# Kernel optimization log

Hardware: AMD Instinct MI355X
Metric: run time of the kernel (lower is better)

## Reference

```python
import jax, jax.numpy as jnp
import numpy as np

MODEL_DIM = 1024
NUM_HEADS = 16
D_K = MODEL_DIM // NUM_HEADS  # 64
MAX_SEQ_LEN = 3200
B, T = 2, 2048
THETA_BASE = 10000.0


def setup_inputs() -> dict:
    key = jax.random.key(0)
    ks = jax.random.split(key, 5)
    scale = 1.0 / np.sqrt(MODEL_DIM)
    x = jax.random.normal(ks[0], (B, T, MODEL_DIM), dtype=jnp.float32)
    wq = jax.random.normal(ks[1], (MODEL_DIM, MODEL_DIM), dtype=jnp.float32) * scale
    wk = jax.random.normal(ks[2], (MODEL_DIM, MODEL_DIM), dtype=jnp.float32) * scale
    wv = jax.random.normal(ks[3], (MODEL_DIM, MODEL_DIM), dtype=jnp.float32) * scale
    wo = jax.random.normal(ks[4], (MODEL_DIM, MODEL_DIM), dtype=jnp.float32) * scale
    bq = jnp.zeros((MODEL_DIM,), jnp.float32)
    bk = jnp.zeros((MODEL_DIM,), jnp.float32)
    bv = jnp.zeros((MODEL_DIM,), jnp.float32)
    bo = jnp.zeros((MODEL_DIM,), jnp.float32)
    # RoPE tables, exactly as precompute_rotation_matrix: theta duplicated
    # adjacently ([t0,t0,t1,t1,...]).
    theta = THETA_BASE ** (jnp.arange(D_K // 2, dtype=jnp.float32) * (-2.0 / D_K))
    ang = jnp.outer(jnp.arange(MAX_SEQ_LEN, dtype=jnp.float32), theta)  # [L, d/2]
    ang = jnp.repeat(ang, 2, axis=-1)  # [L, d]
    return {
        "x": x, "wq": wq, "bq": bq, "wk": wk, "bk": bk,
        "wv": wv, "bv": bv, "wo": wo, "bo": bo,
        "cos": jnp.cos(ang), "sin": jnp.sin(ang),
    }


def reference(x, wq, bq, wk, bk, wv, bv, wo, bo, cos, sin):
    b, t, dm = x.shape
    h, d = NUM_HEADS, dm // NUM_HEADS

    # NOTE: original uses .view(b, h, t, d) directly on [b, t, h*d] (no
    # transpose) — a nonstandard head split we replicate faithfully.
    xq = (x @ wq.T + bq).reshape(b, h, t, d)
    xk = (x @ wk.T + bk).reshape(b, h, t, d)
    xv = (x @ wv.T + bv).reshape(b, h, t, d)

    def rot_half(q):
        # pairs are adjacent (2i, 2i+1): out[2i] = -q[2i+1], out[2i+1] = q[2i]
        q2 = q.reshape(b, h, t, d // 2, 2)
        return jnp.stack([-q2[..., 1], q2[..., 0]], axis=-1).reshape(b, h, t, d)

    # NOTE: original indexes cos/sin at the single position `seq_len`
    # (rotation_matrix_cos[:, :, xq.shape[2], :]), broadcasting one row over
    # all positions — replicated faithfully.
    c = cos[t]  # [d]
    s = sin[t]  # [d]
    xq = xq * c + rot_half(xq) * s
    xk = xk * c + rot_half(xk) * s

    scores = jnp.einsum("bhqd,bhkd->bhqk", xq, xk) / np.sqrt(d)
    p = jax.nn.softmax(scores, axis=-1)  # mask='none', dropout=0.0
    o = jnp.einsum("bhqk,bhkd->bhqd", p, xv)
    o = o.transpose(0, 2, 1, 3).reshape(b, t, dm)  # 'b h t d -> b t (h d)'
    return o @ wo.T + bo
```

## Files before the change

### kernel.cpp

```cpp
#include <hip/hip_runtime.h>

typedef _Float16 half8 __attribute__((ext_vector_type(8)));
typedef __fp16 pkh2 __attribute__((ext_vector_type(2)));
typedef float floatx4 __attribute__((ext_vector_type(4)));

#define AS1 __attribute__((address_space(1)))
#define AS3 __attribute__((address_space(3)))


__global__ __launch_bounds__(256) void convert_kernel(
    const float* __restrict__ x, const float* __restrict__ wq,
    const float* __restrict__ wk, const float* __restrict__ wv,
    const float* __restrict__ wo,
    _Float16* __restrict__ xb, _Float16* __restrict__ wqkv,
    _Float16* __restrict__ wob)
{
    int i = (blockIdx.x * 256 + threadIdx.x) * 4;
    const float* src; _Float16* dst; int off;
    if (i < 4194304)      { src = x;  dst = xb;            off = i; }
    else if (i < 5242880) { src = wq; dst = wqkv;          off = i - 4194304; }
    else if (i < 6291456) { src = wk; dst = wqkv + 1048576; off = i - 5242880; }
    else if (i < 7340032) { src = wv; dst = wqkv + 2097152; off = i - 6291456; }
    else                  { src = wo; dst = wob;           off = i - 7340032; }
    float4 v = *(const float4*)(src + off);
    union { uint2 u; pkh2 h[2]; } o;
    o.h[0] = __builtin_amdgcn_cvt_pkrtz(v.x, v.y);
    o.h[1] = __builtin_amdgcn_cvt_pkrtz(v.z, v.w);
    *(uint2*)(dst + off) = o.u;
}

template<bool QKV, int BM>
__global__ __launch_bounds__(256) void gemm_kernel(
    const _Float16* __restrict__ A, const _Float16* __restrict__ W,
    const float* __restrict__ b0, const float* __restrict__ b1,
    const float* __restrict__ b2,
    const float* __restrict__ cosr, const float* __restrict__ sinr,
    _Float16* __restrict__ O0, _Float16* __restrict__ O1,
    _Float16* __restrict__ O2, float* __restrict__ Of)
{
    constexpr int MT = BM / 32;
    __shared__ __align__(16) _Float16 As[BM * 64];
    __shared__ __align__(16) _Float16 Bs[128 * 64];
    const int tid  = threadIdx.x;
    const int lane = tid & 63, w = tid >> 6;
    const int lrow = lane & 15, quad = lane >> 4;
    const int wr = (w & 1) * (BM / 2), wc = (w >> 1) * 64;
    const int arow0 = blockIdx.x * BM;
    const int brow0 = blockIdx.y * 128;

    const int r8 = lane >> 3;
    const int gcol = ((lane & 7) ^ r8) * 8;

    floatx4 acc[MT][4] = {};

    for (int kk = 0; kk < 1024; kk += 64) {
        __syncthreads();
        for (int u = 0; u < MT; u++) {
            const int row = w * (8 * MT) + u * 8;
            __builtin_amdgcn_global_load_lds(
                (const AS1 unsigned*)(const void*)(A + (size_t)(arow0 + row + r8) * 1024 + kk + gcol),
                (AS3 unsigned*)(void*)(As + row * 64), 16, 0, 0);
        }
        for (int u = 0; u < 4; u++) {
            const int row = w * 32 + u * 8;
            __builtin_amdgcn_global_load_lds(
                (const AS1 unsigned*)(const void*)(W + (size_t)(brow0 + row + r8) * 1024 + kk + gcol),
                (AS3 unsigned*)(void*)(Bs + row * 64), 16, 0, 0);
        }
        __syncthreads();
        for (int ks = 0; ks < 2; ks++) {
            const int swz = ((ks * 4 + quad) ^ (lrow & 7)) * 8;
            half8 af[MT], bf[4];
            for (int mt = 0; mt < MT; mt++)
                af[mt] = *(const half8*)&As[(wr + mt * 16 + lrow) * 64 + swz];
            for (int nt = 0; nt < 4; nt++)
                bf[nt] = *(const half8*)&Bs[(wc + nt * 16 + lrow) * 64 + swz];
            for (int mt = 0; mt < MT; mt++)
                for (int nt = 0; nt < 4; nt++)
                    acc[mt][nt] = __builtin_amdgcn_mfma_f32_16x16x32_f16(
                        af[mt], bf[nt], acc[mt][nt], 0, 0, 0);
        }
    }

    if (QKV) {
        const int seg = blockIdx.y >> 3;
        const float* bias = seg == 0 ? b0 : (seg == 1 ? b1 : b2);
        _Float16* out = seg == 0 ? O0 : (seg == 1 ? O1 : O2);
        const int nbase = (blockIdx.y & 7) * 128 + wc;
        for (int nt = 0; nt < 4; nt++) {
            const int n = nbase + nt * 16 + lrow;
            const float bv = bias[n];
            const int dj = n & 63;
            const float cv = cosr[dj], sv = sinr[dj];
            const bool odd = (n & 1) != 0;
            const int ns = (seg == 1)
                ? ((n & ~56) | ((((n >> 3) ^ (n >> 6)) & 7) << 3))
                : n;
            for (int mt = 0; mt < MT; mt++)
                for (int r = 0; r < 4; r++) {
                    float v = acc[mt][nt][r] + bv;
                    if (seg < 2) {
                        float p = __shfl_xor(v, 1, 64);
                        v = odd ? (v * cv + p * sv) : (v * cv - p * sv);
                    }
                    if (seg == 0) v *= 0.125f;
                    int row = arow0 + wr + mt * 16 + quad * 4 + r;
                    out[row * 1024 + ns] = (_Float16)v;
                }
        }
    } else {
        const int nbase = blockIdx.y * 128 + wc;
        for (int nt = 0; nt < 4; nt++) {
            const int n = nbase + nt * 16 + lrow;
            const float bv = b0[n];
            for (int mt = 0; mt < MT; mt++)
                for (int r = 0; r < 4; r++) {
                    int row = arow0 + wr + mt * 16 + quad * 4 + r;
                    Of[row * 1024 + n] = acc[mt][nt][r] + bv;
                }
        }
    }
}

__global__ __launch_bounds__(256) void vtrans_kernel(
    const _Float16* __restrict__ V, _Float16* __restrict__ VT)
{
    __shared__ __align__(16) _Float16 T[64][72];
    const int tid = threadIdx.x;
    const int kt = blockIdx.x;
    const int bh = blockIdx.y;
    const int bi = bh >> 4, hi = bh & 15;
    const _Float16* Vh = V + (size_t)(bi * 2048 + hi * 128) * 1024 + kt * 4096;
    const int srow = tid >> 3, sblk = tid & 7;
    union { uint4 u; _Float16 h[8]; } a, b;
    a.u = *(const uint4*)(Vh + (2 * srow) * 64 + sblk * 8);
    b.u = *(const uint4*)(Vh + (2 * srow + 1) * 64 + sblk * 8);
    for (int j = 0; j < 8; j++) {
        union { unsigned u; _Float16 h[2]; } pk;
        pk.h[0] = a.h[j]; pk.h[1] = b.h[j];
        *(unsigned*)&T[sblk * 8 + j][2 * srow] = pk.u;
    }
    __syncthreads();
    const int d = tid >> 2, c = tid & 3;
    const int xr = d & 7;
    _Float16* outrow = VT + ((size_t)bh * 64 + d) * 2048 + kt * 64;
    *(uint4*)(outrow + ((2 * c)     ^ xr) * 8) = *(const uint4*)&T[d][c * 16];
    *(uint4*)(outrow + ((2 * c + 1) ^ xr) * 8) = *(const uint4*)&T[d][c * 16 + 8];
}

static __device__ __forceinline__ half8 assemble_p(uint2 a, uint2 b) {
    auto s32x = __builtin_amdgcn_permlane32_swap(a.x, b.x, false, false);
    auto s32y = __builtin_amdgcn_permlane32_swap(a.y, b.y, false, false);
    auto s16x = __builtin_amdgcn_permlane16_swap(s32x[0], s32x[1], false, false);
    auto s16y = __builtin_amdgcn_permlane16_swap(s32y[0], s32y[1], false, false);
    union { uint4 u; half8 h; } r;
    r.u.x = s16x[0];
    r.u.y = s16y[0];
    r.u.z = s16x[1];
    r.u.w = s16y[1];
    return r.h;
}

__global__ __launch_bounds__(512, 4) void attn_kernel(
    const _Float16* __restrict__ Q, const _Float16* __restrict__ K,
    const _Float16* __restrict__ VT, _Float16* __restrict__ O)
{
    __shared__ __align__(16) _Float16 smem[26624];

    const int tid  = threadIdx.x;
    const int g    = tid >> 8;
    const int t8   = tid & 255;
    const int wg   = tid >> 6;
    const int w    = wg & 3;
    const int lane = tid & 63;
    const int lrow = lane & 15, quad = lane >> 4;

    const int bid = blockIdx.x;
    const int bh  = (bid & 7) * 4 + (bid >> 7);
    const int qt  = (bid >> 3) & 15;
    const int bi = bh >> 4, hi = bh & 15;
    const size_t base = (size_t)(bi * 2048 + hi * 128) * 1024;
    const _Float16* Qh  = Q + base;
    const _Float16* Kh  = K + base + (size_t)g * 65536;
    const _Float16* VTh = VT + (size_t)bh * 131072 + g * 1024;

    _Float16* Ksg  = smem + g * 4096;
    _Float16* Vtsg = smem + 8192 + g * 4096;

    half8 qf[2][2];
    for (int nt = 0; nt < 2; nt++)
        for (int ks = 0; ks < 2; ks++)
            qf[nt][ks] = *(const half8*)(Qh + (qt * 128 + w * 32 + nt * 16 + lrow) * 64
                                          + ks * 32 + quad * 8);

    floatx4 oacc[4][2] = {};
    float lsum0 = 0.0f, lsum1 = 0.0f;

    const int srow = t8 >> 3, sblk = t8 & 7;
    const int vd = t8 >> 2;
    const int vq0 = (2 * (t8 & 3)) ^ (vd & 7);
    const int vq1 = vq0 ^ 1;
    const _Float16* vrow = VTh + (size_t)vd * 2048;

    uint4 k0 = *(const uint4*)(Kh + srow * 64 + sblk * 8);
    uint4 k1 = *(const uint4*)(Kh + (srow + 32) * 64 + sblk * 8);
    uint4 v0 = *(const uint4*)(vrow + vq0 * 8);
    uint4 v1 = *(const uint4*)(vrow + vq1 * 8);

    const float LOG2E = 1.44269504f;
    const float OFF   = -8.65617025f;

    for (int ktl = 0; ktl < 16; ktl++) {
        __syncthreads();
        *(uint4*)&Ksg[srow * 64 + sblk * 8]        = k0;
        *(uint4*)&Ksg[(srow + 32) * 64 + sblk * 8] = k1;
        *(uint4*)&Vtsg[vd * 64 + vq0 * 8] = v0;
        *(uint4*)&Vtsg[vd * 64 + vq1 * 8] = v1;
        if (ktl < 15) {
            const _Float16* Kt = Kh + (ktl + 1) * 4096;
            k0 = *(const uint4*)(Kt + srow * 64 + sblk * 8);
            k1 = *(const uint4*)(Kt + (srow + 32) * 64 + sblk * 8);
            const _Float16* Vt = vrow + (ktl + 1) * 64;
            v0 = *(const uint4*)(Vt + vq0 * 8);
            v1 = *(const uint4*)(Vt + vq1 * 8);
        }
        __syncthreads();
        for (int h = 0; h < 2; h++) {
            union { uint2 u; pkh2 h2[2]; } pA[2], pB[2];
            for (int k2 = 0; k2 < 2; k2++) {
                const int kt4 = h * 2 + k2;
                floatx4 s0 = {}, s1 = {};
                for (int ks = 0; ks < 2; ks++) {
                    half8 af = *(const half8*)&Ksg[(kt4 * 16 + lrow) * 64
                                 + (((ks * 4 + quad) ^ (lrow & 7)) * 8)];
                    s0 = __builtin_amdgcn_mfma_f32_16x16x32_f16(af, qf[0][ks], s0, 0, 0, 0);
                    s1 = __builtin_amdgcn_mfma_f32_16x16x32_f16(af, qf[1][ks], s1, 0, 0, 0);
                }
                float p00 = __builtin_amdgcn_exp2f(fmaf(s0[0], LOG2E, OFF));
                float p01 = __builtin_amdgcn_exp2f(fmaf(s0[1], LOG2E, OFF));
                float p02 = __builtin_amdgcn_exp2f(fmaf(s0[2], LOG2E, OFF));
                float p03 = __builtin_amdgcn_exp2f(fmaf(s0[3], LOG2E, OFF));
                float p10 = __builtin_amdgcn_exp2f(fmaf(s1[0], LOG2E, OFF));
                float p11 = __builtin_amdgcn_exp2f(fmaf(s1[1], LOG2E, OFF));
                float p12 = __builtin_amdgcn_exp2f(fmaf(s1[2], LOG2E, OFF));
                float p13 = __builtin_amdgcn_exp2f(fmaf(s1[3], LOG2E, OFF));
                lsum0 += (p00 + p01) + (p02 + p03);
                lsum1 += (p10 + p11) + (p12 + p13);
                pA[k2].h2[0] = __builtin_amdgcn_cvt_pkrtz(p00, p01);
                pA[k2].h2[1] = __builtin_amdgcn_cvt_pkrtz(p02, p03);
                pB[k2].h2[0] = __builtin_amdgcn_cvt_pkrtz(p10, p11);
                pB[k2].h2[1] = __builtin_amdgcn_cvt_pkrtz(p12, p13);
            }
            half8 bf0 = assemble_p(pA[0].u, pA[1].u);
            half8 bf1 = assemble_p(pB[0].u, pB[1].u);
            for (int dt = 0; dt < 4; dt++) {
                half8 av = *(const half8*)&Vtsg[(dt * 16 + lrow) * 64
                              + (((h * 4 + quad) ^ (lrow & 7)) * 8)];
                oacc[dt][0] = __builtin_amdgcn_mfma_f32_16x16x32_f16(av, bf0, oacc[dt][0], 0, 0, 0);
                oacc[dt][1] = __builtin_amdgcn_mfma_f32_16x16x32_f16(av, bf1, oacc[dt][1], 0, 0, 0);
            }
        }
    }
    __syncthreads();

    float* X = (float*)smem;
    float* L = (float*)(smem + 16384);
    if (g == 1) {
        for (int dt = 0; dt < 4; dt++)
            for (int nt = 0; nt < 2; nt++)
                *(floatx4*)&X[((dt * 2 + nt) * 256 + w * 64 + lane) * 4] = oacc[dt][nt];
        L[(w * 64 + lane) * 2]     = lsum0;
        L[(w * 64 + lane) * 2 + 1] = lsum1;
    }
    __syncthreads();
    if (g == 0) {
        for (int dt = 0; dt < 4; dt++)
            for (int nt = 0; nt < 2; nt++)
                oacc[dt][nt] += *(const floatx4*)&X[((dt * 2 + nt) * 256 + w * 64 + lane) * 4];
        lsum0 += L[(w * 64 + lane) * 2];
        lsum1 += L[(w * 64 + lane) * 2 + 1];
        lsum0 += __shfl_xor(lsum0, 16, 64); lsum0 += __shfl_xor(lsum0, 32, 64);
        lsum1 += __shfl_xor(lsum1, 16, 64); lsum1 += __shfl_xor(lsum1, 32, 64);
        const float inv0 = 1.0f / lsum0, inv1 = 1.0f / lsum1;
        _Float16* Es = smem + 17408 + w * 2304;
        for (int dt = 0; dt < 4; dt++) {
            union { uint2 u; pkh2 h2[2]; } a0, a1;
            a0.h2[0] = __builtin_amdgcn_cvt_pkrtz(oacc[dt][0][0] * inv0, oacc[dt][0][1] * inv0);
            a0.h2[1] = __builtin_amdgcn_cvt_pkrtz(oacc[dt][0][2] * inv0, oacc[dt][0][3] * inv0);
            a1.h2[0] = __builtin_amdgcn_cvt_pkrtz(oacc[dt][1][0] * inv1, oacc[dt][1][1] * inv1);
            a1.h2[1] = __builtin_amdgcn_cvt_pkrtz(oacc[dt][1][2] * inv1, oacc[dt][1][3] * inv1);
            *(uint2*)&Es[lrow * 72 + dt * 16 + quad * 4]        = a0.u;
            *(uint2*)&Es[(16 + lrow) * 72 + dt * 16 + quad * 4] = a1.u;
        }
        const int rw = lane >> 1, hf = lane & 1;
        const size_t orow = (size_t)(bi * 2048 + qt * 128 + w * 32 + rw) * 1024
                            + hi * 64 + hf * 32;
        for (int i = 0; i < 4; i++)
            *(uint4*)(O + orow + i * 8) = *(const uint4*)&Es[rw * 72 + hf * 32 + i * 8];
    }
}

extern "C" void kernel_launch(void* const* d_in, const int* in_sizes, int n_in,
                              void* d_out, int out_size, void* d_ws, size_t ws_size,
                              hipStream_t stream) {
    const float* x    = (const float*)d_in[0];
    const float* wq   = (const float*)d_in[1];
    const float* bq   = (const float*)d_in[2];
    const float* wk   = (const float*)d_in[3];
    const float* bk   = (const float*)d_in[4];
    const float* wv   = (const float*)d_in[5];
    const float* bv   = (const float*)d_in[6];
    const float* wo   = (const float*)d_in[7];
    const float* bo   = (const float*)d_in[8];
    const float* cosT = (const float*)d_in[9];
    const float* sinT = (const float*)d_in[10];

    _Float16* ws   = (_Float16*)d_ws;
    _Float16* xb   = ws;
    _Float16* wqkv = xb + 4194304;
    _Float16* wob  = wqkv + 3145728;
    _Float16* Qb   = wob + 1048576;
    _Float16* Kb   = Qb + 4194304;
    _Float16* Vb   = Kb + 4194304;
    _Float16* Ob   = Vb + 4194304;
    _Float16* VTb  = xb;

    convert_kernel<<<8192, 256, 0, stream>>>(x, wq, wk, wv, wo, xb, wqkv, wob);
    gemm_kernel<true, 128><<<dim3(32, 24), 256, 0, stream>>>(
        xb, wqkv, bq, bk, bv, cosT + 2048 * 64, sinT + 2048 * 64,
        Qb, Kb, Vb, nullptr);
    vtrans_kernel<<<dim3(32, 32), 256, 0, stream>>>(Vb, VTb);
    attn_kernel<<<dim3(512), 512, 0, stream>>>(Qb, Kb, VTb, Ob);
    gemm_kernel<false, 64><<<dim3(64, 8), 256, 0, stream>>>(
        Ob, wob, bo, nullptr, nullptr, nullptr, nullptr,
        nullptr, nullptr, nullptr, (float*)d_out);
}
```

Baseline: 207.1 us.

## Double attention key tile to 128 and raise wave priority around MFMA

Each attention loop iteration now stages 128 keys instead of 64 of K and V^T into shared memory, using four register-prefetched loads per thread per operand. This halves the loop trip count and so halves the number of block-wide barriers and load/store phases. It also wraps the QK and PV MFMA sequences in s_setprio so waves issuing matrix work get scheduling priority over the exp/softmax sections. In exchange, shared memory per block grows from 52KB to 64KB and more registers are used for prefetch, which may cut the number of resident blocks per CU.

```diff
diff --git a/kernel.cpp b/kernel.cpp
--- a/kernel.cpp
+++ b/kernel.cpp
@@ -165,7 +165,7 @@
     const _Float16* __restrict__ Q, const _Float16* __restrict__ K,
     const _Float16* __restrict__ VT, _Float16* __restrict__ O)
 {
-    __shared__ __align__(16) _Float16 smem[26624];
+    __shared__ __align__(16) _Float16 smem[32768];
 
     const int tid  = threadIdx.x;
     const int g    = tid >> 8;
@@ -184,8 +184,8 @@
     const _Float16* Kh  = K + base + (size_t)g * 65536;
     const _Float16* VTh = VT + (size_t)bh * 131072 + g * 1024;
 
-    _Float16* Ksg  = smem + g * 4096;
-    _Float16* Vtsg = smem + 8192 + g * 4096;
+    _Float16* Ksg  = smem + g * 8192;
+    _Float16* Vtsg = smem + 16384 + g * 8192;
 
     half8 qf[2][2];
     for (int nt = 0; nt < 2; nt++)
@@ -198,44 +198,47 @@
 
     const int srow = t8 >> 3, sblk = t8 & 7;
     const int vd = t8 >> 2;
-    const int vq0 = (2 * (t8 & 3)) ^ (vd & 7);
-    const int vq1 = vq0 ^ 1;
+    int vb[4];
+    for (int j = 0; j < 4; j++) vb[j] = ((t8 & 3) * 4 + j) ^ (vd & 7);
     const _Float16* vrow = VTh + (size_t)vd * 2048;
 
-    uint4 k0 = *(const uint4*)(Kh + srow * 64 + sblk * 8);
-    uint4 k1 = *(const uint4*)(Kh + (srow + 32) * 64 + sblk * 8);
-    uint4 v0 = *(const uint4*)(vrow + vq0 * 8);
-    uint4 v1 = *(const uint4*)(vrow + vq1 * 8);
+    uint4 kreg[4], vreg[4];
+    for (int i = 0; i < 4; i++)
+        kreg[i] = *(const uint4*)(Kh + (srow + 32 * i) * 64 + sblk * 8);
+    for (int j = 0; j < 4; j++)
+        vreg[j] = *(const uint4*)(vrow + vb[j] * 8);
 
     const float LOG2E = 1.44269504f;
     const float OFF   = -8.65617025f;
 
-    for (int ktl = 0; ktl < 16; ktl++) {
+    for (int ktl = 0; ktl < 8; ktl++) {
         __syncthreads();
-        *(uint4*)&Ksg[srow * 64 + sblk * 8]        = k0;
-        *(uint4*)&Ksg[(srow + 32) * 64 + sblk * 8] = k1;
-        *(uint4*)&Vtsg[vd * 64 + vq0 * 8] = v0;
-        *(uint4*)&Vtsg[vd * 64 + vq1 * 8] = v1;
-        if (ktl < 15) {
-            const _Float16* Kt = Kh + (ktl + 1) * 4096;
-            k0 = *(const uint4*)(Kt + srow * 64 + sblk * 8);
-            k1 = *(const uint4*)(Kt + (srow + 32) * 64 + sblk * 8);
-            const _Float16* Vt = vrow + (ktl + 1) * 64;
-            v0 = *(const uint4*)(Vt + vq0 * 8);
-            v1 = *(const uint4*)(Vt + vq1 * 8);
+        for (int i = 0; i < 4; i++)
+            *(uint4*)&Ksg[(srow + 32 * i) * 64 + sblk * 8] = kreg[i];
+        for (int j = 0; j < 4; j++)
+            *(uint4*)&Vtsg[vd * 128 + vb[j] * 8] = vreg[j];
+        if (ktl < 7) {
+            const _Float16* Kt = Kh + ((ktl + 1) * 128 + srow) * 64 + sblk * 8;
+            for (int i = 0; i < 4; i++)
+                kreg[i] = *(const uint4*)(Kt + i * 32 * 64);
+            const _Float16* Vt = vrow + (ktl + 1) * 128;
+            for (int j = 0; j < 4; j++)
+                vreg[j] = *(const uint4*)(Vt + vb[j] * 8);
         }
         __syncthreads();
-        for (int h = 0; h < 2; h++) {
+        for (int h = 0; h < 4; h++) {
             union { uint2 u; pkh2 h2[2]; } pA[2], pB[2];
             for (int k2 = 0; k2 < 2; k2++) {
                 const int kt4 = h * 2 + k2;
                 floatx4 s0 = {}, s1 = {};
+                __builtin_amdgcn_s_setprio(1);
                 for (int ks = 0; ks < 2; ks++) {
                     half8 af = *(const half8*)&Ksg[(kt4 * 16 + lrow) * 64
                                  + (((ks * 4 + quad) ^ (lrow & 7)) * 8)];
                     s0 = __builtin_amdgcn_mfma_f32_16x16x32_f16(af, qf[0][ks], s0, 0, 0, 0);
                     s1 = __builtin_amdgcn_mfma_f32_16x16x32_f16(af, qf[1][ks], s1, 0, 0, 0);
                 }
+                __builtin_amdgcn_s_setprio(0);
                 float p00 = __builtin_amdgcn_exp2f(fmaf(s0[0], LOG2E, OFF));
                 float p01 = __builtin_amdgcn_exp2f(fmaf(s0[1], LOG2E, OFF));
                 float p02 = __builtin_amdgcn_exp2f(fmaf(s0[2], LOG2E, OFF));
@@ -253,12 +256,15 @@
             }
             half8 bf0 = assemble_p(pA[0].u, pA[1].u);
             half8 bf1 = assemble_p(pB[0].u, pB[1].u);
+            __builtin_amdgcn_s_setprio(1);
             for (int dt = 0; dt < 4; dt++) {
-                half8 av = *(const half8*)&Vtsg[(dt * 16 + lrow) * 64
-                              + (((h * 4 + quad) ^ (lrow & 7)) * 8)];
+                half8 av = *(const half8*)&Vtsg[(dt * 16 + lrow) * 128
+                              + (h >> 1) * 64
+                              + ((((h & 1) * 4 + quad) ^ (lrow & 7)) * 8)];
                 oacc[dt][0] = __builtin_amdgcn_mfma_f32_16x16x32_f16(av, bf0, oacc[dt][0], 0, 0, 0);
                 oacc[dt][1] = __builtin_amdgcn_mfma_f32_16x16x32_f16(av, bf1, oacc[dt][1], 0, 0, 0);
             }
+            __builtin_amdgcn_s_setprio(0);
         }
     }
     __syncthreads();
```

Result: slower. 345.6 us (+66.9%).

## Double-buffer K/V tiles in LDS using direct global-to-LDS loads

Applied to the files above, without the earlier changes.

Replaces the register-staged K/V prefetch, which needed two barriers per iteration, with a two-deep LDS ring filled by global_load_lds. The next tile is issued while the current one is consumed, leaving one barrier per iteration. It also raises wave priority around the MFMA sections with s_setprio. In exchange, LDS use grows to 64KB per block, which may limit how many blocks fit on a CU, and correctness depends on the async LDS writes being complete before the barrier.

```diff
diff --git a/kernel.cpp b/kernel.cpp
--- a/kernel.cpp
+++ b/kernel.cpp
@@ -165,11 +165,10 @@
     const _Float16* __restrict__ Q, const _Float16* __restrict__ K,
     const _Float16* __restrict__ VT, _Float16* __restrict__ O)
 {
-    __shared__ __align__(16) _Float16 smem[26624];
+    __shared__ __align__(16) _Float16 smem[32768];
 
     const int tid  = threadIdx.x;
     const int g    = tid >> 8;
-    const int t8   = tid & 255;
     const int wg   = tid >> 6;
     const int w    = wg & 3;
     const int lane = tid & 63;
@@ -184,8 +183,8 @@
     const _Float16* Kh  = K + base + (size_t)g * 65536;
     const _Float16* VTh = VT + (size_t)bh * 131072 + g * 1024;
 
-    _Float16* Ksg  = smem + g * 4096;
-    _Float16* Vtsg = smem + 8192 + g * 4096;
+    _Float16* Ks0  = smem + g * 16384;
+    _Float16* Vts0 = smem + g * 16384 + 8192;
 
     half8 qf[2][2];
     for (int nt = 0; nt < 2; nt++)
@@ -196,46 +195,48 @@
     floatx4 oacc[4][2] = {};
     float lsum0 = 0.0f, lsum1 = 0.0f;
 
-    const int srow = t8 >> 3, sblk = t8 & 7;
-    const int vd = t8 >> 2;
-    const int vq0 = (2 * (t8 & 3)) ^ (vd & 7);
-    const int vq1 = vq0 ^ 1;
-    const _Float16* vrow = VTh + (size_t)vd * 2048;
-
-    uint4 k0 = *(const uint4*)(Kh + srow * 64 + sblk * 8);
-    uint4 k1 = *(const uint4*)(Kh + (srow + 32) * 64 + sblk * 8);
-    uint4 v0 = *(const uint4*)(vrow + vq0 * 8);
-    uint4 v1 = *(const uint4*)(vrow + vq1 * 8);
+    const _Float16* klsrc = Kh + w * 1024 + lane * 8;
+    const _Float16* vlsrc = VTh + (size_t)(w * 16 + (lane >> 3)) * 2048 + (lane & 7) * 8;
+
+    auto stage = [&](int kt, int b) {
+        const _Float16* ks = klsrc + kt * 4096;
+        _Float16* kd = Ks0 + b * 4096 + w * 1024;
+        __builtin_amdgcn_global_load_lds((const AS1 unsigned*)(const void*)ks,
+                                         (AS3 unsigned*)(void*)kd, 16, 0, 0);
+        __builtin_amdgcn_global_load_lds((const AS1 unsigned*)(const void*)(ks + 512),
+                                         (AS3 unsigned*)(void*)(kd + 512), 16, 0, 0);
+        const _Float16* vs = vlsrc + kt * 64;
+        _Float16* vd = Vts0 + b * 4096 + w * 1024;
+        __builtin_amdgcn_global_load_lds((const AS1 unsigned*)(const void*)vs,
+                                         (AS3 unsigned*)(void*)vd, 16, 0, 0);
+        __builtin_amdgcn_global_load_lds((const AS1 unsigned*)(const void*)(vs + 8 * 2048),
+                                         (AS3 unsigned*)(void*)(vd + 512), 16, 0, 0);
+    };
 
     const float LOG2E = 1.44269504f;
     const float OFF   = -8.65617025f;
 
+    stage(0, 0);
+    __syncthreads();
+
     for (int ktl = 0; ktl < 16; ktl++) {
-        __syncthreads();
-        *(uint4*)&Ksg[srow * 64 + sblk * 8]        = k0;
-        *(uint4*)&Ksg[(srow + 32) * 64 + sblk * 8] = k1;
-        *(uint4*)&Vtsg[vd * 64 + vq0 * 8] = v0;
-        *(uint4*)&Vtsg[vd * 64 + vq1 * 8] = v1;
-        if (ktl < 15) {
-            const _Float16* Kt = Kh + (ktl + 1) * 4096;
-            k0 = *(const uint4*)(Kt + srow * 64 + sblk * 8);
-            k1 = *(const uint4*)(Kt + (srow + 32) * 64 + sblk * 8);
-            const _Float16* Vt = vrow + (ktl + 1) * 64;
-            v0 = *(const uint4*)(Vt + vq0 * 8);
-            v1 = *(const uint4*)(Vt + vq1 * 8);
-        }
-        __syncthreads();
+        const int cur = ktl & 1;
+        if (ktl < 15) stage(ktl + 1, cur ^ 1);
+        const _Float16* Ksg  = Ks0 + cur * 4096;
+        const _Float16* Vtsg = Vts0 + cur * 4096;
         for (int h = 0; h < 2; h++) {
             union { uint2 u; pkh2 h2[2]; } pA[2], pB[2];
             for (int k2 = 0; k2 < 2; k2++) {
                 const int kt4 = h * 2 + k2;
                 floatx4 s0 = {}, s1 = {};
+                __builtin_amdgcn_s_setprio(1);
                 for (int ks = 0; ks < 2; ks++) {
                     half8 af = *(const half8*)&Ksg[(kt4 * 16 + lrow) * 64
                                  + (((ks * 4 + quad) ^ (lrow & 7)) * 8)];
                     s0 = __builtin_amdgcn_mfma_f32_16x16x32_f16(af, qf[0][ks], s0, 0, 0, 0);
                     s1 = __builtin_amdgcn_mfma_f32_16x16x32_f16(af, qf[1][ks], s1, 0, 0, 0);
                 }
+                __builtin_amdgcn_s_setprio(0);
                 float p00 = __builtin_amdgcn_exp2f(fmaf(s0[0], LOG2E, OFF));
                 float p01 = __builtin_amdgcn_exp2f(fmaf(s0[1], LOG2E, OFF));
                 float p02 = __builtin_amdgcn_exp2f(fmaf(s0[2], LOG2E, OFF));
@@ -253,15 +254,17 @@
             }
             half8 bf0 = assemble_p(pA[0].u, pA[1].u);
             half8 bf1 = assemble_p(pB[0].u, pB[1].u);
+            __builtin_amdgcn_s_setprio(1);
             for (int dt = 0; dt < 4; dt++) {
                 half8 av = *(const half8*)&Vtsg[(dt * 16 + lrow) * 64
                               + (((h * 4 + quad) ^ (lrow & 7)) * 8)];
                 oacc[dt][0] = __builtin_amdgcn_mfma_f32_16x16x32_f16(av, bf0, oacc[dt][0], 0, 0, 0);
                 oacc[dt][1] = __builtin_amdgcn_mfma_f32_16x16x32_f16(av, bf1, oacc[dt][1], 0, 0, 0);
             }
-        }
-    }
-    __syncthreads();
+            __builtin_amdgcn_s_setprio(0);
+        }
+        __syncthreads();
+    }
 
     float* X = (float*)smem;
     float* L = (float*)(smem + 16384);
```

Measured after the change: 205.6 us. No clear change (-0.7%).
